# Optimization experiments

Measured on AMD Instinct MI355X. Metric: run time of the kernel, lower is better.

Reference implementation:

```python
import jax, jax.numpy as jnp
import numpy as np

C = 32  # input multiplicity per irrep (0e and 1o)
D = 32  # output multiplicity per irrep


def pe_inputs(x):
    # x: [B, 2, 3, F]; permutation-equivariant pooled channels
    x_self = x
    x_flavor = x.sum(axis=2, keepdims=True) - x_self
    x_nunubar = x.sum(axis=1, keepdims=True) - x_self
    x_all = x.sum(axis=(1, 2), keepdims=True) - x_self - x_flavor - x_nunubar
    x_flavor = x_flavor / (x.shape[2] - 1)
    x_nunubar = x_nunubar / (x.shape[1] - 1)
    x_all = x_all / ((x.shape[1] - 1) * (x.shape[2] - 1))
    return x_self, x_flavor, x_nunubar, x_all


def _split(x):
    # irreps '32x0e + 32x1o': first C scalars, then C vectors flattened (C,3)
    s = x[..., :C]
    v = x[..., C:].reshape(x.shape[:-1] + (C, 3))
    return s, v


def fctp(x1, x2, W):
    # e3nn FullyConnectedTensorProduct('Cx0e+Cx1o', 'Cx0e+Cx1o', 'Dx0e+Dx1o')
    # W: [4, C, C, D] stacked path weights: [ss->s, vv->s, sv->v, vs->v]
    s1, v1 = _split(x1)
    s2, v2 = _split(x2)
    norm = 1.0 / (C * np.sqrt(2.0))  # sqrt(dim(ir_out) / fan), fan = 2*C^2
    inv_sqrt3 = 1.0 / np.sqrt(3.0)   # wigner_3j(1,1,0) = delta_ij/sqrt(3)
    y_s = norm * (jnp.einsum('uvw,...u,...v->...w', W[0], s1, s2)
                  + inv_sqrt3 * jnp.einsum('uvw,...ui,...vi->...w', W[1], v1, v2))
    y_v = norm * (jnp.einsum('uvw,...u,...vk->...wk', W[2], s1, v2)
                  + jnp.einsum('uvw,...uk,...v->...wk', W[3], v1, s2))
    return jnp.concatenate([y_s, y_v.reshape(y_v.shape[:-2] + (3 * D,))], axis=-1)


def setup_inputs() -> dict:
    key = jax.random.key(0)
    ks = jax.random.split(key, 5)
    B = 16384
    x = jax.random.normal(ks[0], (B, 2, 3, C + 3 * C), dtype=jnp.float32)
    W_self = jax.random.normal(ks[1], (4, C, C, D), dtype=jnp.float32)
    W_flavor = jax.random.normal(ks[2], (4, C, C, D), dtype=jnp.float32)
    W_nunubar = jax.random.normal(ks[3], (4, C, C, D), dtype=jnp.float32)
    W_all = jax.random.normal(ks[4], (4, C, C, D), dtype=jnp.float32)
    return {"x": x, "W_self": W_self, "W_flavor": W_flavor,
            "W_nunubar": W_nunubar, "W_all": W_all}


def reference(x, W_self, W_flavor, W_nunubar, W_all):
    xs, xf, xn, xa = pe_inputs(x)
    y = (fctp(xs, xs, W_self)
         + fctp(xf, xf, W_flavor)
         + fctp(xn, xn, W_nunubar)
         + fctp(xa, xa, W_all))
    return y
```

## Files before the change

kernel.cpp:

```cpp
#include <hip/hip_runtime.h>


typedef _Float16 half8  __attribute__((ext_vector_type(8)));
typedef float    f32x16 __attribute__((ext_vector_type(16)));

#define NORM 0.022097086912079608f
#define INV_SQRT3 0.5773502691896258f
#define STR 136

__global__ void prep_kernel(const float* __restrict__ Wa, const float* __restrict__ Wb,
                            const float* __restrict__ Wc, const float* __restrict__ Wd,
                            _Float16* __restrict__ Ball) {
    const float* Ws[4] = {Wa, Wb, Wc, Wd};
    int idx = blockIdx.x * 256 + threadIdx.x;
    if (idx >= 393216) return;
    int e    = idx & 511;
    int frag = idx >> 9;
    int slot = frag % 6;
    int tu   = frag / 6;
    int u = tu & 31;
    int t = tu >> 5;
    int j = e & 7, lane = e >> 3;
    int n = lane & 31, kq = lane >> 5;
    int kh = slot & 1, seg = slot >> 1;
    int v = kh * 16 + kq * 8 + j;
    const float* W = Ws[t];
    float val;
    if (seg == 0)      val = NORM * W[u * 1024 + v * 32 + n];
    else if (seg == 1) val = NORM * INV_SQRT3 * W[32768 + u * 1024 + v * 32 + n];
    else               val = NORM * (W[65536 + u * 1024 + v * 32 + n] +
                                     W[98304 + v * 1024 + u * 32 + n]);
    Ball[idx] = (_Float16)val;
}

__device__ __forceinline__ void gload_lds16(const _Float16* g, _Float16* l) {
    __builtin_amdgcn_global_load_lds(
        (const __attribute__((address_space(1))) unsigned int*)g,
        (__attribute__((address_space(3))) unsigned int*)l, 16, 0, 0);
}

__launch_bounds__(192, 3)
__global__ void petp_main(const float* __restrict__ x,
                          const _Float16* __restrict__ Ball,
                          float* __restrict__ y) {
    __shared__ _Float16 feat[96 * STR];
    __shared__ _Float16 Bst[2][6144];

    const int tid  = threadIdx.x;
    const int wave = tid >> 6;
    const int lane = tid & 63;
    const int mw = lane & 31;
    const int q8 = lane >> 5;
    const int wvu = __builtin_amdgcn_readfirstlane(wave);

    f32x16 acc_s;
    f32x16 acc_v[3];
#pragma unroll
    for (int r = 0; r < 16; ++r) {
        acc_s[r] = 0.f; acc_v[0][r] = 0.f; acc_v[1][r] = 0.f; acc_v[2][r] = 0.f;
    }

    const int wg = blockIdx.x;
    const float* xg = x + (size_t)wg * (96 * 128);

#pragma unroll 1
    for (int t = 0; t < 4; ++t) {
        const _Float16* Bt = Ball + t * 98304;

#pragma unroll
        for (int i = 0; i < 4; ++i) {
            int fi = wvu * 4 + i;
            gload_lds16(Bt + fi * 512 + lane * 8, &Bst[0][fi * 512]);
        }

#pragma unroll 1
        for (int it = 0; it < 11; ++it) {
            int item = it * 192 + tid;
            if (item < 2048) {
                int b = item >> 7;
                int c = item & 127;
                const float* bp = xg + b * 768 + c;
                float v00 = bp[0],   v01 = bp[128], v02 = bp[256];
                float v10 = bp[384], v11 = bp[512], v12 = bp[640];
                float rs0 = v00 + v01 + v02, rs1 = v10 + v11 + v12;
                float cs0 = v00 + v10, cs1 = v01 + v11, cs2 = v02 + v12;
                float tot = rs0 + rs1;
                float xv[6] = {v00, v01, v02, v10, v11, v12};
                float rs[2] = {rs0, rs1};
                float cs[3] = {cs0, cs1, cs2};
                int row;
                if (c < 32) row = c;
                else { int cc = c - 32; row = 32 + (cc % 3) * 32 + (cc / 3); }
                _Float16* fp = feat + row;
#pragma unroll
                for (int p6 = 0; p6 < 6; ++p6) {
                    int i = p6 / 3, j = p6 % 3;
                    float xvv = xv[p6];
                    float f;
                    if      (t == 0) f = xvv;
                    else if (t == 1) f = (rs[i] - xvv) * 0.5f;
                    else if (t == 2) f = cs[j] - xvv;
                    else             f = (tot - rs[i] - cs[j] + xvv) * 0.5f;
                    fp[(b * 6 + p6) * STR] = (_Float16)f;
                }
            }
        }
        asm volatile("s_waitcnt vmcnt(0)" ::: "memory");
        __syncthreads();

        const _Float16* frow = feat + (wave * 32 + mw) * STR;
        half8 sl_s[2];
        half8 sl_v[2][3];
#pragma unroll
        for (int kh = 0; kh < 2; ++kh) {
            sl_s[kh] = *(const half8*)(frow + kh * 16 + q8 * 8);
#pragma unroll
            for (int i = 0; i < 3; ++i)
                sl_v[kh][i] = *(const half8*)(frow + 32 + i * 32 + kh * 16 + q8 * 8);
        }

        half8 bcS, bcG0, bcG1, bcG2;

#pragma unroll
        for (int c = 0; c < 16; ++c) {
            if (c < 15) {
#pragma unroll
                for (int i = 0; i < 4; ++i) {
                    int fi = wvu * 4 + i;
                    gload_lds16(Bt + ((c + 1) * 12 + fi) * 512 + lane * 8,
                                &Bst[(c + 1) & 1][fi * 512]);
                }
            }
            if ((c & 3) == 0) {
                const int cku = c >> 2;
                bcS  = *(const half8*)(frow + cku * 8);
                bcG0 = *(const half8*)(frow + 32 + cku * 8);
                bcG1 = *(const half8*)(frow + 64 + cku * 8);
                bcG2 = *(const half8*)(frow + 96 + cku * 8);
            }
            const _Float16* BstC = &Bst[c & 1][0];
#pragma unroll
            for (int ul = 0; ul < 2; ++ul) {
                const int uu = (c * 2 + ul) & 7;
                const _Float16* F = BstC + ul * 3072 + lane * 8;
                half8 bA0 = *(const half8*)(F);
                half8 bA1 = *(const half8*)(F + 512);
                half8 bG0 = *(const half8*)(F + 1024);
                half8 bG1 = *(const half8*)(F + 1536);
                half8 bV0 = *(const half8*)(F + 2048);
                half8 bV1 = *(const half8*)(F + 2560);
                _Float16 su = bcS[uu];
                _Float16 g0 = bcG0[uu], g1 = bcG1[uu], g2 = bcG2[uu];

                half8 af;
                af = sl_s[0] * su;
                acc_s = __builtin_amdgcn_mfma_f32_32x32x16_f16(af, bA0, acc_s, 0, 0, 0);
                af = sl_s[1] * su;
                acc_s = __builtin_amdgcn_mfma_f32_32x32x16_f16(af, bA1, acc_s, 0, 0, 0);
                af = sl_v[0][0] * g0 + sl_v[0][1] * g1 + sl_v[0][2] * g2;
                acc_s = __builtin_amdgcn_mfma_f32_32x32x16_f16(af, bG0, acc_s, 0, 0, 0);
                af = sl_v[1][0] * g0 + sl_v[1][1] * g1 + sl_v[1][2] * g2;
                acc_s = __builtin_amdgcn_mfma_f32_32x32x16_f16(af, bG1, acc_s, 0, 0, 0);
#pragma unroll
                for (int kc = 0; kc < 3; ++kc) {
                    half8 af0 = sl_v[0][kc] * su;
                    acc_v[kc] = __builtin_amdgcn_mfma_f32_32x32x16_f16(af0, bV0, acc_v[kc], 0, 0, 0);
                    half8 af1 = sl_v[1][kc] * su;
                    acc_v[kc] = __builtin_amdgcn_mfma_f32_32x32x16_f16(af1, bV1, acc_v[kc], 0, 0, 0);
                }
            }
            asm volatile("s_waitcnt vmcnt(0)" ::: "memory");
            __syncthreads();
        }
    }

    float* yg = y + (size_t)wg * (96 * 128);
    const int pb = wave * 32 + q8 * 4;
#pragma unroll
    for (int r = 0; r < 16; ++r) {
        int pos = pb + (r & 3) + 8 * (r >> 2);
        float* yp = yg + pos * 128;
        __builtin_nontemporal_store(acc_s[r], yp + mw);
        __builtin_nontemporal_store(acc_v[0][r], yp + 32 + 3 * mw + 0);
        __builtin_nontemporal_store(acc_v[1][r], yp + 32 + 3 * mw + 1);
        __builtin_nontemporal_store(acc_v[2][r], yp + 32 + 3 * mw + 2);
    }
}

extern "C" void kernel_launch(void* const* d_in, const int* in_sizes, int n_in,
                              void* d_out, int out_size, void* d_ws, size_t ws_size,
                              hipStream_t stream) {
    const float* x  = (const float*)d_in[0];
    const float* Wa = (const float*)d_in[1];
    const float* Wb = (const float*)d_in[2];
    const float* Wc = (const float*)d_in[3];
    const float* Wd = (const float*)d_in[4];
    float* y = (float*)d_out;

    _Float16* Ball = (_Float16*)d_ws;

    int nbatch = in_sizes[0] / 768;
    int nwg = nbatch / 16;

    prep_kernel<<<1536, 256, 0, stream>>>(Wa, Wb, Wc, Wd, Ball);
    petp_main<<<nwg, 192, 0, stream>>>(x, Ball, y);
}
```

Before: 260.3 us.

## Triple-buffer weight staging with partial vmcnt waits and vectorize prep writes

The main kernel moves from a double to a triple LDS buffer for the weight fragments. It prefetches two chunks ahead, waits with vmcnt(4) instead of draining all loads, and uses one barrier per chunk instead of two sync points. MFMA sections run at raised priority via s_setprio. The prep kernel now writes each weight fragment as one 16-byte vector with 8x fewer threads. The larger LDS footprint lowers the occupancy hint from 3 to 2 blocks, and the vmcnt(4) count assumes exactly four outstanding global loads per wave at each wait, which relies on the compiler's load ordering.

Measured after the change: 264.8 us. Within noise of the previous version (+1.7%).

```diff
diff --git a/kernel.cpp b/kernel.cpp
--- a/kernel.cpp
+++ b/kernel.cpp
@@ -11,26 +11,29 @@
 __global__ void prep_kernel(const float* __restrict__ Wa, const float* __restrict__ Wb,
                             const float* __restrict__ Wc, const float* __restrict__ Wd,
                             _Float16* __restrict__ Ball) {
-    const float* Ws[4] = {Wa, Wb, Wc, Wd};
     int idx = blockIdx.x * 256 + threadIdx.x;
-    if (idx >= 393216) return;
-    int e    = idx & 511;
-    int frag = idx >> 9;
+    if (idx >= 49152) return;
+    int lane = idx & 63;
+    int frag = idx >> 6;
     int slot = frag % 6;
     int tu   = frag / 6;
-    int u = tu & 31;
-    int t = tu >> 5;
-    int j = e & 7, lane = e >> 3;
+    int u = tu & 31, t = tu >> 5;
     int n = lane & 31, kq = lane >> 5;
     int kh = slot & 1, seg = slot >> 1;
-    int v = kh * 16 + kq * 8 + j;
+    const float* Ws[4] = {Wa, Wb, Wc, Wd};
     const float* W = Ws[t];
-    float val;
-    if (seg == 0)      val = NORM * W[u * 1024 + v * 32 + n];
-    else if (seg == 1) val = NORM * INV_SQRT3 * W[32768 + u * 1024 + v * 32 + n];
-    else               val = NORM * (W[65536 + u * 1024 + v * 32 + n] +
-                                     W[98304 + v * 1024 + u * 32 + n]);
-    Ball[idx] = (_Float16)val;
+    half8 out;
+#pragma unroll
+    for (int j = 0; j < 8; ++j) {
+        int v = kh * 16 + kq * 8 + j;
+        float val;
+        if (seg == 0)      val = NORM * W[u * 1024 + v * 32 + n];
+        else if (seg == 1) val = NORM * INV_SQRT3 * W[32768 + u * 1024 + v * 32 + n];
+        else               val = NORM * (W[65536 + u * 1024 + v * 32 + n] +
+                                         W[98304 + v * 1024 + u * 32 + n]);
+        out[j] = (_Float16)val;
+    }
+    *(half8*)(Ball + (size_t)frag * 512 + lane * 8) = out;
 }
 
 __device__ __forceinline__ void gload_lds16(const _Float16* g, _Float16* l) {
@@ -39,12 +42,12 @@
         (__attribute__((address_space(3))) unsigned int*)l, 16, 0, 0);
 }
 
-__launch_bounds__(192, 3)
+__launch_bounds__(192, 2)
 __global__ void petp_main(const float* __restrict__ x,
                           const _Float16* __restrict__ Ball,
                           float* __restrict__ y) {
     __shared__ _Float16 feat[96 * STR];
-    __shared__ _Float16 Bst[2][6144];
+    __shared__ _Float16 Bst[3][6144];
 
     const int tid  = threadIdx.x;
     const int wave = tid >> 6;
@@ -65,13 +68,17 @@
 
 #pragma unroll 1
     for (int t = 0; t < 4; ++t) {
+        __builtin_amdgcn_s_barrier();
+
         const _Float16* Bt = Ball + t * 98304;
 
 #pragma unroll
-        for (int i = 0; i < 4; ++i) {
-            int fi = wvu * 4 + i;
-            gload_lds16(Bt + fi * 512 + lane * 8, &Bst[0][fi * 512]);
-        }
+        for (int cc = 0; cc < 2; ++cc)
+#pragma unroll
+            for (int i = 0; i < 4; ++i) {
+                int fi = wvu * 4 + i;
+                gload_lds16(Bt + (cc * 12 + fi) * 512 + lane * 8, &Bst[cc][fi * 512]);
+            }
 
 #pragma unroll 1
         for (int it = 0; it < 11; ++it) {
@@ -90,7 +97,7 @@
                 float cs[3] = {cs0, cs1, cs2};
                 int row;
                 if (c < 32) row = c;
-                else { int cc = c - 32; row = 32 + (cc % 3) * 32 + (cc / 3); }
+                else { int cc2 = c - 32; row = 32 + (cc2 % 3) * 32 + (cc2 / 3); }
                 _Float16* fp = feat + row;
 #pragma unroll
                 for (int p6 = 0; p6 < 6; ++p6) {
@@ -105,30 +112,38 @@
                 }
             }
         }
-        asm volatile("s_waitcnt vmcnt(0)" ::: "memory");
-        __syncthreads();
-
-        const _Float16* frow = feat + (wave * 32 + mw) * STR;
+
         half8 sl_s[2];
         half8 sl_v[2][3];
-#pragma unroll
-        for (int kh = 0; kh < 2; ++kh) {
-            sl_s[kh] = *(const half8*)(frow + kh * 16 + q8 * 8);
-#pragma unroll
-            for (int i = 0; i < 3; ++i)
-                sl_v[kh][i] = *(const half8*)(frow + 32 + i * 32 + kh * 16 + q8 * 8);
-        }
-
         half8 bcS, bcG0, bcG1, bcG2;
+        const _Float16* frow = feat + (wave * 32 + mw) * STR;
 
 #pragma unroll
         for (int c = 0; c < 16; ++c) {
-            if (c < 15) {
+            if (c == 0)
+                asm volatile("s_waitcnt vmcnt(4) lgkmcnt(0)" ::: "memory");
+            else if (c < 15)
+                asm volatile("s_waitcnt vmcnt(4)" ::: "memory");
+            else
+                asm volatile("s_waitcnt vmcnt(0)" ::: "memory");
+            __builtin_amdgcn_s_barrier();
+
+            if (c < 14) {
 #pragma unroll
                 for (int i = 0; i < 4; ++i) {
                     int fi = wvu * 4 + i;
-                    gload_lds16(Bt + ((c + 1) * 12 + fi) * 512 + lane * 8,
-                                &Bst[(c + 1) & 1][fi * 512]);
+                    gload_lds16(Bt + ((c + 2) * 12 + fi) * 512 + lane * 8,
+                                &Bst[(c + 2) % 3][fi * 512]);
+                }
+            }
+
+            if (c == 0) {
+#pragma unroll
+                for (int kh = 0; kh < 2; ++kh) {
+                    sl_s[kh] = *(const half8*)(frow + kh * 16 + q8 * 8);
+#pragma unroll
+                    for (int i = 0; i < 3; ++i)
+                        sl_v[kh][i] = *(const half8*)(frow + 32 + i * 32 + kh * 16 + q8 * 8);
                 }
             }
             if ((c & 3) == 0) {
@@ -138,7 +153,9 @@
                 bcG1 = *(const half8*)(frow + 64 + cku * 8);
                 bcG2 = *(const half8*)(frow + 96 + cku * 8);
             }
-            const _Float16* BstC = &Bst[c & 1][0];
+
+            const _Float16* BstC = &Bst[c % 3][0];
+            __builtin_amdgcn_s_setprio(1);
 #pragma unroll
             for (int ul = 0; ul < 2; ++ul) {
                 const int uu = (c * 2 + ul) & 7;
@@ -169,8 +186,7 @@
                     acc_v[kc] = __builtin_amdgcn_mfma_f32_32x32x16_f16(af1, bV1, acc_v[kc], 0, 0, 0);
                 }
             }
-            asm volatile("s_waitcnt vmcnt(0)" ::: "memory");
-            __syncthreads();
+            __builtin_amdgcn_s_setprio(0);
         }
     }
 
@@ -202,6 +218,6 @@
     int nbatch = in_sizes[0] / 768;
     int nwg = nbatch / 16;
 
-    prep_kernel<<<1536, 256, 0, stream>>>(Wa, Wb, Wc, Wd, Ball);
+    prep_kernel<<<192, 256, 0, stream>>>(Wa, Wb, Wc, Wd, Ball);
     petp_main<<<nwg, 192, 0, stream>>>(x, Ball, y);
 }
```
